# Optimization experiments

Hardware: AMD Instinct MI355X
Metric: run time of the kernel (lower is better)

The kernel has to match this reference:

```python
import jax, jax.numpy as jnp
import numpy as np

H = 2048          # hidden_size
L_CACHE = 3       # depthwise conv kernel size
BATCH, SEQ = 2, 4096


def setup_inputs() -> dict:
    key = jax.random.key(0)
    k1, k2, k3, k4 = jax.random.split(key, 4)
    hidden_states = jax.random.normal(k1, (BATCH, SEQ, H), dtype=jnp.float32)
    # torch nn.Linear weights: [out_features, in_features]
    W_in = jax.random.normal(k2, (3 * H, H), dtype=jnp.float32) * (1.0 / np.sqrt(H))
    W_out = jax.random.normal(k3, (H, H), dtype=jnp.float32) * (1.0 / np.sqrt(H))
    # torch depthwise Conv1d weight: [H, 1, L]
    W_conv = jax.random.normal(k4, (H, 1, L_CACHE), dtype=jnp.float32) * (1.0 / np.sqrt(L_CACHE))
    return {"hidden_states": hidden_states, "W_in": W_in, "W_conv": W_conv, "W_out": W_out}


def reference(hidden_states, W_in, W_conv, W_out):
    # in_proj: [B,S,H] @ [H,3H] -> [B,S,3H]
    BCx = jnp.einsum('bsh,oh->bso', hidden_states, W_in)
    Bg, Cg, x = jnp.split(BCx, 3, axis=-1)   # each [B,S,H]
    Bx = Bg * x                              # gate before conv
    # depthwise causal conv over sequence: operate in NCH layout
    Bx_nch = jnp.transpose(Bx, (0, 2, 1))    # [B,H,S]
    conv_out = jax.lax.conv_general_dilated(
        Bx_nch, W_conv,
        window_strides=(1,),
        padding=[(L_CACHE - 1, 0)],          # causal: left pad only
        dimension_numbers=('NCH', 'OIH', 'NCH'),
        feature_group_count=H,
    )                                        # [B,H,S]
    y = Cg * jnp.transpose(conv_out, (0, 2, 1))  # C gating, back to [B,S,H]
    return jnp.einsum('bsh,oh->bso', y, W_out)   # out_proj
```

## Files before the change

kernel.cpp:

```cpp
#include <hip/hip_runtime.h>
#include <hip/hip_fp16.h>


typedef _Float16 f16x8 __attribute__((ext_vector_type(8)));
typedef float    f32x4 __attribute__((ext_vector_type(4)));

#define GLD_LDS16(gsrc, sdst) \
  __builtin_amdgcn_global_load_lds((const __attribute__((address_space(1))) void*)(gsrc), \
                                   (__attribute__((address_space(3))) void*)(sdst), 16, 0, 0)

#define VMCNT4 asm volatile("s_waitcnt vmcnt(4)" ::: "memory")
#define VMCNT0 asm volatile("s_waitcnt vmcnt(0)" ::: "memory")
#define LGKM0  asm volatile("s_waitcnt lgkmcnt(0)" ::: "memory")
#define BAR    __builtin_amdgcn_s_barrier()

__global__ __launch_bounds__(256) void cvt_f32_f16(const float* __restrict__ in,
                                                   _Float16* __restrict__ out, int n) {
  int i = blockIdx.x * 256 + threadIdx.x;
  int base = i * 8;
  if (base >= n) return;
  const float4* p = reinterpret_cast<const float4*>(in) + i * 2;
  float4 a = p[0], b = p[1];
  f16x8 o;
  o[0] = (_Float16)a.x; o[1] = (_Float16)a.y; o[2] = (_Float16)a.z; o[3] = (_Float16)a.w;
  o[4] = (_Float16)b.x; o[5] = (_Float16)b.y; o[6] = (_Float16)b.z; o[7] = (_Float16)b.w;
  *reinterpret_cast<f16x8*>(out + base) = o;
}

__global__ __launch_bounds__(256) void conv_gate(const _Float16* __restrict__ BCx,
                                                 const float* __restrict__ Wc,
                                                 _Float16* __restrict__ Y) {
  const int h0 = threadIdx.x * 8;
  const int r0 = blockIdx.x * 8;
  const int s0 = r0 & 4095;

  float w0[8], w1[8], w2[8];
#pragma unroll
  for (int j = 0; j < 8; ++j) {
    w0[j] = Wc[(h0 + j) * 3 + 0];
    w1[j] = Wc[(h0 + j) * 3 + 1];
    w2[j] = Wc[(h0 + j) * 3 + 2];
  }

  float bxm2[8] = {}, bxm1[8] = {};
  if (s0 != 0) {
    const _Float16* pm2 = BCx + (size_t)(r0 - 2) * 6144 + h0;
    const _Float16* pm1 = BCx + (size_t)(r0 - 1) * 6144 + h0;
    f16x8 bg2 = *reinterpret_cast<const f16x8*>(pm2);
    f16x8 xx2 = *reinterpret_cast<const f16x8*>(pm2 + 4096);
    f16x8 bg1 = *reinterpret_cast<const f16x8*>(pm1);
    f16x8 xx1 = *reinterpret_cast<const f16x8*>(pm1 + 4096);
#pragma unroll
    for (int j = 0; j < 8; ++j) {
      bxm2[j] = (float)bg2[j] * (float)xx2[j];
      bxm1[j] = (float)bg1[j] * (float)xx1[j];
    }
  }

  for (int i = 0; i < 8; ++i) {
    const _Float16* pr = BCx + (size_t)(r0 + i) * 6144 + h0;
    f16x8 bg = *reinterpret_cast<const f16x8*>(pr);
    f16x8 cg = *reinterpret_cast<const f16x8*>(pr + 2048);
    f16x8 xx = *reinterpret_cast<const f16x8*>(pr + 4096);
    f16x8 o;
#pragma unroll
    for (int j = 0; j < 8; ++j) {
      float bx   = (float)bg[j] * (float)xx[j];
      float conv = w0[j] * bxm2[j] + w1[j] * bxm1[j] + w2[j] * bx;
      o[j] = (_Float16)((float)cg[j] * conv);
      bxm2[j] = bxm1[j];
      bxm1[j] = bx;
    }
    *reinterpret_cast<f16x8*>(Y + (size_t)(r0 + i) * 2048 + h0) = o;
  }
}

__device__ __forceinline__ void ldA(f16x8 (&af)[4][2], const _Float16* p, int base, int ak0, int ak1) {
#pragma unroll
  for (int i = 0; i < 4; ++i) {
    af[i][0] = *(const f16x8*)(p + base + i * 1024 + ak0);
    af[i][1] = *(const f16x8*)(p + base + i * 1024 + ak1);
  }
}
__device__ __forceinline__ void ldB(f16x8 (&bf)[2][2], const _Float16* p, int base, int ak0, int ak1) {
#pragma unroll
  for (int j = 0; j < 2; ++j) {
    bf[j][0] = *(const f16x8*)(p + base + j * 1024 + ak0);
    bf[j][1] = *(const f16x8*)(p + base + j * 1024 + ak1);
  }
}
template <int QM, int QN>
__device__ __forceinline__ void mfmaQ(f32x4 (&acc)[8][4], const f16x8 (&af)[4][2], const f16x8 (&bf)[2][2]) {
  __builtin_amdgcn_s_setprio(1);
#pragma unroll
  for (int i = 0; i < 4; ++i)
#pragma unroll
    for (int j = 0; j < 2; ++j)
#pragma unroll
      for (int ks = 0; ks < 2; ++ks)
        acc[QM * 4 + i][QN * 2 + j] =
            __builtin_amdgcn_mfma_f32_16x16x32_f16(af[i][ks], bf[j][ks], acc[QM * 4 + i][QN * 2 + j], 0, 0, 0);
  __builtin_amdgcn_s_setprio(0);
}

template <typename CT>
__global__ __launch_bounds__(512, 2) void gemm8p(const _Float16* __restrict__ Ag,
                                                 const _Float16* __restrict__ Bg,
                                                 CT* __restrict__ Cg,
                                                 int N, int K, int nbn) {
  __shared__ __align__(16) char smem[131072];
  const int tid = threadIdx.x, lane = tid & 63, w = tid >> 6;
  const int wr = w >> 2, wc = w & 3;

  const int nwg = (int)gridDim.x, q8 = nwg >> 3;
  const int swz = ((int)blockIdx.x & 7) * q8 + ((int)blockIdx.x >> 3);
  const int bm = (swz / nbn) << 8, bn = (swz % nbn) << 8;

  _Float16* const A0 = (_Float16*)(smem);
  _Float16* const B0 = (_Float16*)(smem + 32768);
  _Float16* const A1 = (_Float16*)(smem + 65536);
  _Float16* const B1 = (_Float16*)(smem + 98304);

  const int rr = tid >> 3;
  const int sCol = ((tid & 7) ^ (rr & 7)) * 8;
  const _Float16* aSrc = Ag + (size_t)(bm + rr) * K + sCol;
  const _Float16* bSrc = Bg + (size_t)(bn + (rr >> 5) * 64 + (rr & 31)) * K + sCol;

  const int ak0 = ((lane >> 4) ^ (lane & 7)) * 8;
  const int ak1 = (((lane >> 4) + 4) ^ (lane & 7)) * 8;
  const int aRB = (wr * 128 + (lane & 15)) * 64;
  const int bRB = (wc * 32 + (lane & 15)) * 64;

  const int nt = K >> 6;

#define STG_A(NBO, kt, u) GLD_LDS16(aSrc + (size_t)(u) * 64 * K + (kt) * 64, \
                                    smem + (NBO) + (u) * 8192 + tid * 16)
#define STG_B(NBO, kt, u) GLD_LDS16(bSrc + (size_t)(((u) & 1) * 128 + ((u) >> 1) * 32) * K + (kt) * 64, \
                                    smem + (NBO) + 32768 + (u) * 8192 + tid * 16)

  f16x8 af[4][2], bf[2][2];
  f32x4 acc[8][4] = {};

  STG_A(0, 0, 0); STG_A(0, 0, 2);
  STG_B(0, 0, 0); STG_B(0, 0, 1);
  STG_B(0, 0, 2); STG_B(0, 0, 3);
  STG_A(0, 0, 1); STG_A(0, 0, 3);
  VMCNT4; BAR;

#define TILE(AB, BB, NBO, t)                                       \
  {                                                                \
    const int tn = ((t) + 1 < nt) ? (t) + 1 : nt - 1;              \
                                                  \
    ldA(af, AB, aRB, ak0, ak1);                                    \
    ldB(bf, BB, bRB, ak0, ak1);                                    \
    STG_A(NBO, tn, 0); STG_A(NBO, tn, 2);                          \
    BAR; LGKM0;                                                    \
    mfmaQ<0, 0>(acc, af, bf);                                      \
    VMCNT4; BAR;                                                   \
                                                  \
    ldB(bf, BB, bRB + 8192, ak0, ak1);                             \
    STG_B(NBO, tn, 0); STG_B(NBO, tn, 1);                          \
    BAR; LGKM0;                                                    \
    mfmaQ<0, 1>(acc, af, bf);                                      \
    VMCNT4; BAR;                                                   \
                                                  \
    ldA(af, AB, aRB + 4096, ak0, ak1);                             \
    STG_B(NBO, tn, 2); STG_B(NBO, tn, 3);                          \
    BAR; LGKM0;                                                    \
    mfmaQ<1, 1>(acc, af, bf);                                      \
    BAR;                                                           \
                                \
    ldB(bf, BB, bRB, ak0, ak1);                                    \
    STG_A(NBO, tn, 1); STG_A(NBO, tn, 3);                          \
    BAR; LGKM0;                                                    \
    mfmaQ<1, 0>(acc, af, bf);                                      \
    VMCNT4; BAR;                                                   \
  }

  for (int t = 0; t < nt; t += 2) {
    TILE(A0, B0, 65536, t);
    TILE(A1, B1, 0, t + 1);
  }
  VMCNT0;

  const int rb = bm + wr * 128 + ((lane >> 4) << 2);
  const int cb = bn + wc * 64 + (lane & 15);
#pragma unroll
  for (int mi = 0; mi < 8; ++mi)
#pragma unroll
    for (int nj = 0; nj < 4; ++nj) {
      f32x4 v = acc[mi][nj];
#pragma unroll
      for (int rg = 0; rg < 4; ++rg)
        Cg[(size_t)(rb + mi * 16 + rg) * N + cb + nj * 16] = (CT)v[rg];
    }
#undef TILE
#undef STG_A
#undef STG_B
}

extern "C" void kernel_launch(void* const* d_in, const int* in_sizes, int n_in,
                              void* d_out, int out_size, void* d_ws, size_t ws_size,
                              hipStream_t stream) {
  const float* X  = (const float*)d_in[0];
  const float* Wi = (const float*)d_in[1];
  const float* Wc = (const float*)d_in[2];
  const float* Wo = (const float*)d_in[3];
  float* out = (float*)d_out;

  char* ws = (char*)d_ws;
  _Float16* Xh   = (_Float16*)(ws);
  _Float16* Wih  = (_Float16*)(ws + 33554432);
  _Float16* Woh  = (_Float16*)(ws + 58720256);
  _Float16* BCxh = (_Float16*)(ws + 67108864);
  _Float16* Yh   = (_Float16*)(ws + 167772160);
  (void)ws_size; (void)in_sizes; (void)n_in; (void)out_size;

  cvt_f32_f16<<<dim3(16777216 / 2048), 256, 0, stream>>>(X,  Xh,  16777216);
  cvt_f32_f16<<<dim3(12582912 / 2048), 256, 0, stream>>>(Wi, Wih, 12582912);
  cvt_f32_f16<<<dim3( 4194304 / 2048), 256, 0, stream>>>(Wo, Woh,  4194304);

  gemm8p<_Float16><<<dim3(768), 512, 0, stream>>>(Xh, Wih, BCxh, 6144, 2048, 24);

  conv_gate<<<dim3(1024), 256, 0, stream>>>(BCxh, Wc, Yh);

  gemm8p<float><<<dim3(256), 512, 0, stream>>>(Yh, Woh, out, 2048, 2048, 8);
}
```

Before: 314.1 us.

## Switch GEMM to 32x32x16 MFMA tiles and tighten phase synchronization

Result: slower. 345.8 us (+10.1%).

```diff
diff --git a/kernel.cpp b/kernel.cpp
--- a/kernel.cpp
+++ b/kernel.cpp
@@ -2,8 +2,9 @@
 #include <hip/hip_fp16.h>
 
 
-typedef _Float16 f16x8 __attribute__((ext_vector_type(8)));
-typedef float    f32x4 __attribute__((ext_vector_type(4)));
+typedef _Float16 f16x8  __attribute__((ext_vector_type(8)));
+typedef float    f32x4  __attribute__((ext_vector_type(4)));
+typedef float    f32x16 __attribute__((ext_vector_type(16)));
 
 #define GLD_LDS16(gsrc, sdst) \
   __builtin_amdgcn_global_load_lds((const __attribute__((address_space(1))) void*)(gsrc), \
@@ -13,6 +14,7 @@
 #define VMCNT0 asm volatile("s_waitcnt vmcnt(0)" ::: "memory")
 #define LGKM0  asm volatile("s_waitcnt lgkmcnt(0)" ::: "memory")
 #define BAR    __builtin_amdgcn_s_barrier()
+#define SCHED0 __builtin_amdgcn_sched_barrier(0)
 
 __global__ __launch_bounds__(256) void cvt_f32_f16(const float* __restrict__ in,
                                                    _Float16* __restrict__ out, int n) {
@@ -75,31 +77,30 @@
   }
 }
 
-__device__ __forceinline__ void ldA(f16x8 (&af)[4][2], const _Float16* p, int base, int ak0, int ak1) {
-#pragma unroll
-  for (int i = 0; i < 4; ++i) {
-    af[i][0] = *(const f16x8*)(p + base + i * 1024 + ak0);
-    af[i][1] = *(const f16x8*)(p + base + i * 1024 + ak1);
-  }
-}
-__device__ __forceinline__ void ldB(f16x8 (&bf)[2][2], const _Float16* p, int base, int ak0, int ak1) {
-#pragma unroll
-  for (int j = 0; j < 2; ++j) {
-    bf[j][0] = *(const f16x8*)(p + base + j * 1024 + ak0);
-    bf[j][1] = *(const f16x8*)(p + base + j * 1024 + ak1);
-  }
+__device__ __forceinline__ void ldA32(f16x8 (&af)[2][4], const _Float16* p, int base,
+                                      const int (&akc)[4]) {
+#pragma unroll
+  for (int f = 0; f < 2; ++f)
+#pragma unroll
+    for (int ks = 0; ks < 4; ++ks)
+      af[f][ks] = *(const f16x8*)(p + base + f * 2048 + akc[ks]);
+}
+__device__ __forceinline__ void ldB32(f16x8 (&bf)[4], const _Float16* p, int base,
+                                      const int (&akc)[4]) {
+#pragma unroll
+  for (int ks = 0; ks < 4; ++ks)
+    bf[ks] = *(const f16x8*)(p + base + akc[ks]);
 }
 template <int QM, int QN>
-__device__ __forceinline__ void mfmaQ(f32x4 (&acc)[8][4], const f16x8 (&af)[4][2], const f16x8 (&bf)[2][2]) {
+__device__ __forceinline__ void mfmaQ32(f32x16 (&acc)[4][2], const f16x8 (&af)[2][4],
+                                        const f16x8 (&bf)[4]) {
   __builtin_amdgcn_s_setprio(1);
 #pragma unroll
-  for (int i = 0; i < 4; ++i)
-#pragma unroll
-    for (int j = 0; j < 2; ++j)
-#pragma unroll
-      for (int ks = 0; ks < 2; ++ks)
-        acc[QM * 4 + i][QN * 2 + j] =
-            __builtin_amdgcn_mfma_f32_16x16x32_f16(af[i][ks], bf[j][ks], acc[QM * 4 + i][QN * 2 + j], 0, 0, 0);
+  for (int ks = 0; ks < 4; ++ks)
+#pragma unroll
+    for (int f = 0; f < 2; ++f)
+      acc[QM * 2 + f][QN] =
+          __builtin_amdgcn_mfma_f32_32x32x16_f16(af[f][ks], bf[ks], acc[QM * 2 + f][QN], 0, 0, 0);
   __builtin_amdgcn_s_setprio(0);
 }
 
@@ -126,10 +127,12 @@
   const _Float16* aSrc = Ag + (size_t)(bm + rr) * K + sCol;
   const _Float16* bSrc = Bg + (size_t)(bn + (rr >> 5) * 64 + (rr & 31)) * K + sCol;
 
-  const int ak0 = ((lane >> 4) ^ (lane & 7)) * 8;
-  const int ak1 = (((lane >> 4) + 4) ^ (lane & 7)) * 8;
-  const int aRB = (wr * 128 + (lane & 15)) * 64;
-  const int bRB = (wc * 32 + (lane & 15)) * 64;
+  int akc[4];
+#pragma unroll
+  for (int ks = 0; ks < 4; ++ks)
+    akc[ks] = ((ks * 2 + (lane >> 5)) ^ (lane & 7)) * 8;
+  const int aRB = (wr * 128 + (lane & 31)) * 64;
+  const int bRB = (wc * 32 + (lane & 31)) * 64;
 
   const int nt = K >> 6;
 
@@ -138,8 +141,9 @@
 #define STG_B(NBO, kt, u) GLD_LDS16(bSrc + (size_t)(((u) & 1) * 128 + ((u) >> 1) * 32) * K + (kt) * 64, \
                                     smem + (NBO) + 32768 + (u) * 8192 + tid * 16)
 
-  f16x8 af[4][2], bf[2][2];
-  f32x4 acc[8][4] = {};
+  f16x8 af[2][4];
+  f16x8 bf[4];
+  f32x16 acc[4][2] = {};
 
   STG_A(0, 0, 0); STG_A(0, 0, 2);
   STG_B(0, 0, 0); STG_B(0, 0, 1);
@@ -150,31 +154,27 @@
 #define TILE(AB, BB, NBO, t)                                       \
   {                                                                \
     const int tn = ((t) + 1 < nt) ? (t) + 1 : nt - 1;              \
-                                                  \
-    ldA(af, AB, aRB, ak0, ak1);                                    \
-    ldB(bf, BB, bRB, ak0, ak1);                                    \
+                                                \
+    ldA32(af, AB, aRB, akc);                                       \
+    ldB32(bf, BB, bRB, akc);                                       \
     STG_A(NBO, tn, 0); STG_A(NBO, tn, 2);                          \
-    BAR; LGKM0;                                                    \
-    mfmaQ<0, 0>(acc, af, bf);                                      \
-    VMCNT4; BAR;                                                   \
-                                                  \
-    ldB(bf, BB, bRB + 8192, ak0, ak1);                             \
+    VMCNT4; BAR; LGKM0; SCHED0;                                    \
+    mfmaQ32<0, 0>(acc, af, bf);                                    \
+                                                \
+    ldB32(bf, BB, bRB + 8192, akc);                                \
     STG_B(NBO, tn, 0); STG_B(NBO, tn, 1);                          \
-    BAR; LGKM0;                                                    \
-    mfmaQ<0, 1>(acc, af, bf);                                      \
-    VMCNT4; BAR;                                                   \
-                                                  \
-    ldA(af, AB, aRB + 4096, ak0, ak1);                             \
+    VMCNT4; BAR; LGKM0; SCHED0;                                    \
+    mfmaQ32<0, 1>(acc, af, bf);                                    \
+                                \
+    ldA32(af, AB, aRB + 4096, akc);                                \
     STG_B(NBO, tn, 2); STG_B(NBO, tn, 3);                          \
-    BAR; LGKM0;                                                    \
-    mfmaQ<1, 1>(acc, af, bf);                                      \
-    BAR;                                                           \
-                                \
-    ldB(bf, BB, bRB, ak0, ak1);                                    \
+    BAR; LGKM0; SCHED0;                                            \
+    mfmaQ32<1, 1>(acc, af, bf);                                    \
+                              \
+    ldB32(bf, BB, bRB, akc);                                       \
     STG_A(NBO, tn, 1); STG_A(NBO, tn, 3);                          \
-    BAR; LGKM0;                                                    \
-    mfmaQ<1, 0>(acc, af, bf);                                      \
-    VMCNT4; BAR;                                                   \
+    VMCNT4; BAR; LGKM0; SCHED0;                                    \
+    mfmaQ32<1, 0>(acc, af, bf);                                    \
   }
 
   for (int t = 0; t < nt; t += 2) {
@@ -183,16 +183,18 @@
   }
   VMCNT0;
 
-  const int rb = bm + wr * 128 + ((lane >> 4) << 2);
-  const int cb = bn + wc * 64 + (lane & 15);
-#pragma unroll
-  for (int mi = 0; mi < 8; ++mi)
-#pragma unroll
-    for (int nj = 0; nj < 4; ++nj) {
-      f32x4 v = acc[mi][nj];
-#pragma unroll
-      for (int rg = 0; rg < 4; ++rg)
-        Cg[(size_t)(rb + mi * 16 + rg) * N + cb + nj * 16] = (CT)v[rg];
+  const int cb0 = bn + wc * 64 + (lane & 31);
+  const int rb0 = bm + wr * 128 + 4 * (lane >> 5);
+#pragma unroll
+  for (int mf = 0; mf < 4; ++mf)
+#pragma unroll
+    for (int nf = 0; nf < 2; ++nf) {
+      f32x16 v = acc[mf][nf];
+      const int col = cb0 + nf * 32;
+      const int rb  = rb0 + mf * 32;
+#pragma unroll
+      for (int rg = 0; rg < 16; ++rg)
+        Cg[(size_t)(rb + (rg & 3) + 8 * (rg >> 2)) * N + col] = (CT)v[rg];
     }
 #undef TILE
 #undef STG_A
```

## Software-pipeline LDS fragment loads with MFMA and merge conversion kernels

Applied to the files above, without the earlier changes.

After: 297.7 us. -5.2%, faster.

```diff
diff --git a/kernel.cpp b/kernel.cpp
--- a/kernel.cpp
+++ b/kernel.cpp
@@ -10,21 +10,31 @@
                                    (__attribute__((address_space(3))) void*)(sdst), 16, 0, 0)
 
 #define VMCNT4 asm volatile("s_waitcnt vmcnt(4)" ::: "memory")
+#define VMCNT2 asm volatile("s_waitcnt vmcnt(2)" ::: "memory")
 #define VMCNT0 asm volatile("s_waitcnt vmcnt(0)" ::: "memory")
 #define LGKM0  asm volatile("s_waitcnt lgkmcnt(0)" ::: "memory")
 #define BAR    __builtin_amdgcn_s_barrier()
-
-__global__ __launch_bounds__(256) void cvt_f32_f16(const float* __restrict__ in,
-                                                   _Float16* __restrict__ out, int n) {
-  int i = blockIdx.x * 256 + threadIdx.x;
-  int base = i * 8;
-  if (base >= n) return;
-  const float4* p = reinterpret_cast<const float4*>(in) + i * 2;
+#define SCHED0 __builtin_amdgcn_sched_barrier(0)
+
+__global__ __launch_bounds__(256) void cvt_all(const float* __restrict__ X,
+                                               const float* __restrict__ Wi,
+                                               const float* __restrict__ Wo,
+                                               _Float16* __restrict__ Xh,
+                                               _Float16* __restrict__ Wih,
+                                               _Float16* __restrict__ Woh) {
+  int base = (blockIdx.x * 256 + threadIdx.x) * 8;
+  const float* src;
+  _Float16* dst;
+  int off;
+  if (base < 16777216)      { src = X;  dst = Xh;  off = base; }
+  else if (base < 29360128) { src = Wi; dst = Wih; off = base - 16777216; }
+  else                      { src = Wo; dst = Woh; off = base - 29360128; }
+  const float4* p = reinterpret_cast<const float4*>(src + off);
   float4 a = p[0], b = p[1];
   f16x8 o;
   o[0] = (_Float16)a.x; o[1] = (_Float16)a.y; o[2] = (_Float16)a.z; o[3] = (_Float16)a.w;
   o[4] = (_Float16)b.x; o[5] = (_Float16)b.y; o[6] = (_Float16)b.z; o[7] = (_Float16)b.w;
-  *reinterpret_cast<f16x8*>(out + base) = o;
+  *reinterpret_cast<f16x8*>(dst + off) = o;
 }
 
 __global__ __launch_bounds__(256) void conv_gate(const _Float16* __restrict__ BCx,
@@ -145,41 +155,43 @@
   STG_B(0, 0, 0); STG_B(0, 0, 1);
   STG_B(0, 0, 2); STG_B(0, 0, 3);
   STG_A(0, 0, 1); STG_A(0, 0, 3);
-  VMCNT4; BAR;
-
-#define TILE(AB, BB, NBO, t)                                       \
+  VMCNT0; BAR;
+  ldA(af, A0, aRB, ak0, ak1);
+  ldB(bf, B0, bRB, ak0, ak1);
+
+#define TILE(AB, BB, ABn, BBn, NBO, t)                             \
   {                                                                \
     const int tn = ((t) + 1 < nt) ? (t) + 1 : nt - 1;              \
-                                                  \
-    ldA(af, AB, aRB, ak0, ak1);                                    \
-    ldB(bf, BB, bRB, ak0, ak1);                                    \
+               \
+    LGKM0; SCHED0;                                                 \
+    mfmaQ<0, 0>(acc, af, bf);                                      \
+    ldB(bf, BB, bRB + 8192, ak0, ak1);                             \
     STG_A(NBO, tn, 0); STG_A(NBO, tn, 2);                          \
-    BAR; LGKM0;                                                    \
-    mfmaQ<0, 0>(acc, af, bf);                                      \
+    STG_B(NBO, tn, 0); STG_B(NBO, tn, 1);                          \
     VMCNT4; BAR;                                                   \
-                                                  \
-    ldB(bf, BB, bRB + 8192, ak0, ak1);                             \
-    STG_B(NBO, tn, 0); STG_B(NBO, tn, 1);                          \
-    BAR; LGKM0;                                                    \
+                    \
+    LGKM0; SCHED0;                                                 \
     mfmaQ<0, 1>(acc, af, bf);                                      \
-    VMCNT4; BAR;                                                   \
-                                                  \
     ldA(af, AB, aRB + 4096, ak0, ak1);                             \
     STG_B(NBO, tn, 2); STG_B(NBO, tn, 3);                          \
-    BAR; LGKM0;                                                    \
+    BAR;                                                           \
+            \
+    LGKM0; SCHED0;                                                 \
     mfmaQ<1, 1>(acc, af, bf);                                      \
-    BAR;                                                           \
-                                \
     ldB(bf, BB, bRB, ak0, ak1);                                    \
     STG_A(NBO, tn, 1); STG_A(NBO, tn, 3);                          \
-    BAR; LGKM0;                                                    \
+    VMCNT4; BAR;                                                   \
+      \
+    LGKM0; SCHED0;                                                 \
     mfmaQ<1, 0>(acc, af, bf);                                      \
-    VMCNT4; BAR;                                                   \
+    ldA(af, ABn, aRB, ak0, ak1);                                   \
+    ldB(bf, BBn, bRB, ak0, ak1);                                   \
+    VMCNT2; BAR;                                                   \
   }
 
   for (int t = 0; t < nt; t += 2) {
-    TILE(A0, B0, 65536, t);
-    TILE(A1, B1, 0, t + 1);
+    TILE(A0, B0, A1, B1, 65536, t);
+    TILE(A1, B1, A0, B0, 0, t + 1);
   }
   VMCNT0;
 
@@ -216,9 +228,7 @@
   _Float16* Yh   = (_Float16*)(ws + 167772160);
   (void)ws_size; (void)in_sizes; (void)n_in; (void)out_size;
 
-  cvt_f32_f16<<<dim3(16777216 / 2048), 256, 0, stream>>>(X,  Xh,  16777216);
-  cvt_f32_f16<<<dim3(12582912 / 2048), 256, 0, stream>>>(Wi, Wih, 12582912);
-  cvt_f32_f16<<<dim3( 4194304 / 2048), 256, 0, stream>>>(Wo, Woh,  4194304);
+  cvt_all<<<dim3(16384), 256, 0, stream>>>(X, Wi, Wo, Xh, Wih, Woh);
 
   gemm8p<_Float16><<<dim3(768), 512, 0, stream>>>(Xh, Wih, BCxh, 6144, 2048, 24);
 
```
